# Kernel optimization log

Hardware: AMD Instinct MI355X
Metric: run time of the kernel (lower is better)

The kernel has to match this reference:

```python
import jax, jax.numpy as jnp
import numpy as np

N_NODES = 100000
N_EDGES = 1280000
N_REL = 8
DIM = 64
N_LAYERS = 2
N_TGT = 50000


def setup_inputs() -> dict:
    key = jax.random.key(0)
    ks = jax.random.split(key, 8)
    x_idx = jnp.arange(N_NODES, dtype=jnp.int64) if jax.config.jax_enable_x64 else jnp.arange(N_NODES, dtype=jnp.int32)
    edge_index = jax.random.randint(ks[0], (2, N_EDGES), 0, N_NODES)
    edge_type = jax.random.randint(ks[1], (N_EDGES,), 0, N_REL)
    target_edge_index = jax.random.randint(ks[2], (2, N_TGT), 0, N_NODES)
    # xavier-ish scales to keep activations stable through relu stack
    node_emb = jax.random.normal(ks[3], (N_NODES, DIM), dtype=jnp.float32) * 0.1
    weight = jax.random.normal(ks[4], (N_LAYERS, N_REL, DIM, DIM), dtype=jnp.float32) * (1.0 / np.sqrt(DIM))
    root = jax.random.normal(ks[5], (N_LAYERS, DIM, DIM), dtype=jnp.float32) * (1.0 / np.sqrt(DIM))
    bias = jax.random.normal(ks[6], (N_LAYERS, DIM), dtype=jnp.float32) * 0.01
    return {"x_idx": x_idx, "edge_index": edge_index, "edge_type": edge_type,
            "target_edge_index": target_edge_index, "node_emb": node_emb,
            "weight": weight, "root": root, "bias": bias}


def reference(x_idx, edge_index, edge_type, target_edge_index, node_emb, weight, root, bias):
    # RGCN forward: x = node_emb[x_idx]; L x (FastRGCNConv + relu); edge dot-product score.
    x = node_emb[x_idx]                       # [N, D]
    src, dst = edge_index[0], edge_index[1]   # messages flow src -> dst (PyG source_to_target)
    n = x.shape[0]
    # in-degree for 'mean' aggregation (zero-degree nodes get 0, guard div)
    deg = jax.ops.segment_sum(jnp.ones((src.shape[0],), dtype=x.dtype), dst, num_segments=n)
    inv_deg = (1.0 / jnp.maximum(deg, 1.0))[:, None]  # [N, 1]
    n_layers = weight.shape[0]
    for l in range(n_layers):
        # transform every node by every relation, then gather per edge (FastRGCNConv math)
        h = jnp.einsum('ni,rio->rno', x, weight[l])   # [R, N, D]
        msg = h[edge_type, src]                       # [E, D]
        agg = jax.ops.segment_sum(msg, dst, num_segments=n) * inv_deg  # mean aggr [N, D]
        x = jax.nn.relu(agg + x @ root[l] + bias[l])
    s, t = target_edge_index[0], target_edge_index[1]
    return jnp.sum(x[s] * x[t], axis=-1)              # [T]
```

## Files before the change

### kernel.cpp

```cpp
#include <hip/hip_runtime.h>
#include <hip/hip_bf16.h>

#define DIM 64
#define NREL 8
#define KTOT 576

typedef __bf16 bf16x8 __attribute__((ext_vector_type(8)));
typedef __bf16 bf16x4 __attribute__((ext_vector_type(4)));
typedef float  f32x4  __attribute__((ext_vector_type(4)));

__global__ __launch_bounds__(256) void histgather_kernel(const int* __restrict__ dst,
                                                         const int* __restrict__ et,
                                                         int* __restrict__ deg8,
                                                         int* __restrict__ eoff,
                                                         const int* __restrict__ x_idx,
                                                         const float* __restrict__ emb,
                                                         __bf16* __restrict__ xb0,
                                                         __bf16* __restrict__ hbuf,
                                                         int* __restrict__ srcs,
                                                         int N, int E, int epad_cap) {
    int i = blockIdx.x * 256 + threadIdx.x;
    if (i < N * DIM) {
        int n = i >> 6;
        int c = i & 63;
        xb0[i] = (__bf16)emb[(size_t)x_idx[n] * DIM + c];
    }
    if (i < DIM) {
        hbuf[(size_t)N * NREL * DIM + i] = (__bf16)0.f;
    }
    if (i < epad_cap) srcs[i] = N * NREL;
    if (i < E) eoff[i] = atomicAdd(&deg8[dst[i] * 8 + et[i]], 1);
}

__global__ __launch_bounds__(256) void scan1_kernel(const int* __restrict__ deg8,
                                                    int* __restrict__ offs,
                                                    int* __restrict__ bsum,
                                                    float* __restrict__ invdeg, int N) {
    __shared__ int sd[256];
    int tid = threadIdx.x;
    int d = blockIdx.x * 256 + tid;
    int vpad = 0;
    if (d < N) {
        int vtrue = 0;
#pragma unroll
        for (int r = 0; r < NREL; ++r) vtrue += deg8[d * 8 + r];
        vpad = (vtrue + 3) & ~3;
        invdeg[d] = 1.0f / fmaxf((float)vtrue, 1.0f);
    }
    sd[tid] = vpad;
    __syncthreads();
#pragma unroll
    for (int off = 1; off < 256; off <<= 1) {
        int t = (tid >= off) ? sd[tid - off] : 0;
        __syncthreads();
        sd[tid] += t;
        __syncthreads();
    }
    if (d < N) offs[d] = sd[tid] - vpad;
    if (tid == 255) bsum[blockIdx.x] = sd[255];
}

__global__ __launch_bounds__(512) void scan2wcat_kernel(int* __restrict__ bsum, int nb,
                                                        const float* __restrict__ weight,
                                                        const float* __restrict__ root,
                                                        __bf16* __restrict__ Wt2, int L) {
    if (blockIdx.x == 0) {
        __shared__ int sd[512];
        int tid = threadIdx.x;
        int v = (tid < nb) ? bsum[tid] : 0;
        sd[tid] = v;
        __syncthreads();
#pragma unroll
        for (int off = 1; off < 512; off <<= 1) {
            int t = (tid >= off) ? sd[tid - off] : 0;
            __syncthreads();
            sd[tid] += t;
            __syncthreads();
        }
        if (tid < nb) bsum[tid] = sd[tid] - v;
    } else {
        int idx = (blockIdx.x - 1) * 512 + threadIdx.x;
        int total = L * KTOT * DIM;
        if (idx >= total) return;
        int l = idx / (KTOT * DIM);
        int rem = idx - l * (KTOT * DIM);
        int row = rem / DIM;
        int ch = rem - row * DIM;
        float w;
        if (row < 512) {
            int r = row >> 6, c = row & 63;
            w = weight[(((l * 8 + r) * 64) + ch) * 64 + c];
        } else {
            w = root[(l * 64 + ch) * 64 + (row - 512)];
        }
        Wt2[idx] = (__bf16)w;
    }
}

__global__ __launch_bounds__(256) void rpbuild_kernel(const int* __restrict__ deg8,
                                                      const int* __restrict__ offs,
                                                      const int* __restrict__ bsum,
                                                      int* __restrict__ rp,
                                                      int N) {
    int d = blockIdx.x * 256 + threadIdx.x;
    if (d >= N) return;
    int base = offs[d] + bsum[blockIdx.x];
    int run = 0;
#pragma unroll
    for (int r = 0; r < NREL; ++r) {
        rp[d * 8 + r] = base + run;
        run += deg8[d * 8 + r];
    }
    if (d == N - 1) rp[(size_t)N * 8] = base + ((run + 3) & ~3);
}

__global__ __launch_bounds__(256) void bucket_kernel(const int* __restrict__ src,
                                                     const int* __restrict__ dst,
                                                     const int* __restrict__ et,
                                                     const int* __restrict__ rp,
                                                     const int* __restrict__ eoff,
                                                     int* __restrict__ srcs, int E) {
    int i = blockIdx.x * 256 + threadIdx.x;
    int half = (E + 1) >> 1;
    if (i >= half) return;
    int iB = i + half;
    bool hasB = iB < E;
    int etA = et[i];
    int etB = hasB ? et[iB] : 0;
    int cellA = dst[i] * 8 + etA;
    int cellB = hasB ? dst[iB] * 8 + etB : 0;
    int rA = rp[cellA];
    int rB = hasB ? rp[cellB] : 0;
    int oA = eoff[i];
    int oB = hasB ? eoff[iB] : 0;
    int sA = src[i];
    int sB = hasB ? src[iB] : 0;
    srcs[rA + oA] = sA * NREL + etA;
    if (hasB) srcs[rB + oB] = sB * NREL + etB;
}

__global__ __launch_bounds__(256) void transform_kernel(const __bf16* __restrict__ xin,
                                                        const __bf16* __restrict__ Wt2,
                                                        __bf16* __restrict__ h, int N) {
    int wave = threadIdx.x >> 6;
    int lane = threadIdx.x & 63;
    int l15 = lane & 15;
    int lg  = lane >> 4;

    bf16x8 afrag[8][2];
#pragma unroll
    for (int p = 0; p < 8; ++p) {
        const __bf16* wrow = Wt2 + (size_t)(p * 64 + 16 * wave + l15) * DIM + lg * 8;
        afrag[p][0] = *reinterpret_cast<const bf16x8*>(wrow);
        afrag[p][1] = *reinterpret_cast<const bf16x8*>(wrow + 32);
    }
    int cb = 16 * wave + 4 * lg;

    int ntiles = (N + 15) >> 4;
    for (int tile = blockIdx.x; tile < ntiles; tile += gridDim.x) {
        int n = tile * 16 + l15;
        int nc = (n < N) ? n : (N - 1);
        const __bf16* xrow = xin + (size_t)nc * DIM + lg * 8;
        bf16x8 bv0 = *reinterpret_cast<const bf16x8*>(xrow);
        bf16x8 bv1 = *reinterpret_cast<const bf16x8*>(xrow + 32);

#pragma unroll
        for (int p = 0; p < 8; ++p) {
            f32x4 acc = (f32x4){0.f, 0.f, 0.f, 0.f};
            acc = __builtin_amdgcn_mfma_f32_16x16x32_bf16(afrag[p][0], bv0, acc, 0, 0, 0);
            acc = __builtin_amdgcn_mfma_f32_16x16x32_bf16(afrag[p][1], bv1, acc, 0, 0, 0);
            if (n < N) {
                bf16x4 hv;
#pragma unroll
                for (int i = 0; i < 4; ++i) hv[i] = (__bf16)acc[i];
                *reinterpret_cast<bf16x4*>(h + (size_t)n * (NREL * DIM) + p * 64 + cb) = hv;
            }
        }
    }
}

__global__ __launch_bounds__(256) void aggroot_kernel(const __bf16* __restrict__ h,
                                                      const __bf16* __restrict__ xin,
                                                      const int* __restrict__ srcs,
                                                      const int* __restrict__ rp,
                                                      const float* __restrict__ invdeg,
                                                      const __bf16* __restrict__ Wt2,
                                                      const float* __restrict__ bias_l,
                                                      __bf16* __restrict__ xout, int N) {
    __shared__ __align__(16) float S16[16][68];
    int wave = threadIdx.x >> 6;
    int lane = threadIdx.x & 63;
    int l15 = lane & 15;
    int lg  = lane >> 4;
    const int SENT = N * NREL;

    bf16x8 ar0, ar1;
    {
        const __bf16* wrow = Wt2 + (size_t)(512 + 16 * wave + l15) * DIM + lg * 8;
        ar0 = *reinterpret_cast<const bf16x8*>(wrow);
        ar1 = *reinterpret_cast<const bf16x8*>(wrow + 32);
    }
    int cbase = 16 * wave + 4 * lg;
    f32x4 bias4 = *reinterpret_cast<const f32x4*>(bias_l + cbase);

    int tile = blockIdx.x;

#pragma unroll
    for (int rr = 0; rr < 4; ++rr) {
        int d0 = tile * 16 + wave * 4 + rr;
        if (d0 >= N) d0 = N - 1;
        int d = __builtin_amdgcn_readfirstlane(d0);
        int qb = rp[d * 8];
        int qe = rp[d * 8 + 8];
        float acc = 0.f;
        for (int q = qb; q < qe; q += 16) {
            int rem = qe - q;
            int4 sa = *reinterpret_cast<const int4*>(srcs + q);
            int4 sb = *reinterpret_cast<const int4*>(srcs + q + 4);
            int4 sc = *reinterpret_cast<const int4*>(srcs + q + 8);
            int4 sd = *reinterpret_cast<const int4*>(srcs + q + 12);
            bool vb = rem >= 8, vc = rem >= 12, vd = rem >= 16;
            int i0 = sa.x,              i1 = sa.y,              i2 = sa.z,              i3 = sa.w;
            int i4 = vb ? sb.x : SENT,  i5 = vb ? sb.y : SENT,  i6 = vb ? sb.z : SENT,  i7 = vb ? sb.w : SENT;
            int i8 = vc ? sc.x : SENT,  i9 = vc ? sc.y : SENT,  iA = vc ? sc.z : SENT,  iB = vc ? sc.w : SENT;
            int iC = vd ? sd.x : SENT,  iD = vd ? sd.y : SENT,  iE = vd ? sd.z : SENT,  iF = vd ? sd.w : SENT;
            float v0 = (float)h[(size_t)i0 * DIM + lane];
            float v1 = (float)h[(size_t)i1 * DIM + lane];
            float v2 = (float)h[(size_t)i2 * DIM + lane];
            float v3 = (float)h[(size_t)i3 * DIM + lane];
            float v4 = (float)h[(size_t)i4 * DIM + lane];
            float v5 = (float)h[(size_t)i5 * DIM + lane];
            float v6 = (float)h[(size_t)i6 * DIM + lane];
            float v7 = (float)h[(size_t)i7 * DIM + lane];
            float v8 = (float)h[(size_t)i8 * DIM + lane];
            float v9 = (float)h[(size_t)i9 * DIM + lane];
            float vA = (float)h[(size_t)iA * DIM + lane];
            float vB = (float)h[(size_t)iB * DIM + lane];
            float vC = (float)h[(size_t)iC * DIM + lane];
            float vD = (float)h[(size_t)iD * DIM + lane];
            float vE = (float)h[(size_t)iE * DIM + lane];
            float vF = (float)h[(size_t)iF * DIM + lane];
            acc += (((v0 + v1) + (v2 + v3)) + ((v4 + v5) + (v6 + v7)))
                 + (((v8 + v9) + (vA + vB)) + ((vC + vD) + (vE + vF)));
        }
        S16[wave * 4 + rr][lane] = acc * invdeg[d];
    }
    __syncthreads();

    int n = tile * 16 + l15;
    int nc = (n < N) ? n : (N - 1);
    const __bf16* xrow = xin + (size_t)nc * DIM + lg * 8;
    bf16x8 bv0 = *reinterpret_cast<const bf16x8*>(xrow);
    bf16x8 bv1 = *reinterpret_cast<const bf16x8*>(xrow + 32);
    f32x4 acc = (f32x4){0.f, 0.f, 0.f, 0.f};
    acc = __builtin_amdgcn_mfma_f32_16x16x32_bf16(ar0, bv0, acc, 0, 0, 0);
    acc = __builtin_amdgcn_mfma_f32_16x16x32_bf16(ar1, bv1, acc, 0, 0, 0);

    if (n < N) {
        f32x4 ag = *reinterpret_cast<const f32x4*>(&S16[l15][cbase]);
        bf16x4 hv;
#pragma unroll
        for (int i = 0; i < 4; ++i)
            hv[i] = (__bf16)fmaxf(acc[i] + ag[i] + bias4[i], 0.f);
        *reinterpret_cast<bf16x4*>(xout + (size_t)n * DIM + cbase) = hv;
    }
}

__global__ __launch_bounds__(256) void score_kernel(const __bf16* __restrict__ xb,
                                                    const int* __restrict__ s,
                                                    const int* __restrict__ t,
                                                    float* __restrict__ out, int T) {
    int i = blockIdx.x * 4 + (threadIdx.x >> 6);
    if (i >= T) return;
    int lane = threadIdx.x & 63;
    float p = (float)xb[(size_t)s[i] * DIM + lane] * (float)xb[(size_t)t[i] * DIM + lane];
#pragma unroll
    for (int off = 32; off > 0; off >>= 1) p += __shfl_down(p, off, 64);
    if (lane == 0) out[i] = p;
}

extern "C" void kernel_launch(void* const* d_in, const int* in_sizes, int n_in,
                              void* d_out, int out_size, void* d_ws, size_t ws_size,
                              hipStream_t stream) {
    const int*   x_idx  = (const int*)d_in[0];
    const int*   eidx   = (const int*)d_in[1];
    const int*   etyp   = (const int*)d_in[2];
    const int*   tidx   = (const int*)d_in[3];
    const float* emb    = (const float*)d_in[4];
    const float* weight = (const float*)d_in[5];
    const float* root   = (const float*)d_in[6];
    const float* bias   = (const float*)d_in[7];

    int N = in_sizes[0];
    int E = in_sizes[2];
    int T = in_sizes[3] / 2;
    int L = in_sizes[5] / (NREL * DIM * DIM);

    const int* src = eidx;
    const int* dst = eidx + E;
    const int* ts  = tidx;
    const int* tt  = tidx + T;
    float* out = (float*)d_out;

    int epad_cap = E + 3 * N + 64;

    char* p = (char*)d_ws;
    auto alloc = [&](size_t bytes) -> void* {
        void* r = (void*)p;
        p += (bytes + 255) & ~(size_t)255;
        return r;
    };
    __bf16* hbuf    = (__bf16*)alloc(((size_t)N * NREL + 1) * DIM * sizeof(__bf16));
    __bf16* xb0     = (__bf16*)alloc((size_t)N * DIM * sizeof(__bf16));
    __bf16* xb1     = (__bf16*)alloc((size_t)N * DIM * sizeof(__bf16));
    __bf16* Wt2     = (__bf16*)alloc((size_t)L * KTOT * DIM * sizeof(__bf16));
    int*    srcs    = (int*)   alloc((size_t)epad_cap * sizeof(int));
    int*    eoff    = (int*)   alloc((size_t)E * sizeof(int));
    int*    deg8    = (int*)   alloc((size_t)N * 8 * sizeof(int));
    int*    rp      = (int*)   alloc(((size_t)N * 8 + 1) * sizeof(int));
    int*    offs    = (int*)   alloc((size_t)N * sizeof(int));
    float*  invdeg  = (float*) alloc((size_t)N * sizeof(float));
    int*    bsum    = (int*)   alloc(1024 * sizeof(int));

    int nb = (N + 255) / 256;
    int ntiles = (N + 15) / 16;

    hipMemsetAsync(deg8, 0, (size_t)N * 8 * sizeof(int), stream);
    histgather_kernel<<<((size_t)N * DIM + 255) / 256, 256, 0, stream>>>(
        dst, etyp, deg8, eoff, x_idx, emb, xb0, hbuf, srcs, N, E, epad_cap);
    scan1_kernel<<<nb, 256, 0, stream>>>(deg8, offs, bsum, invdeg, N);
    {
        int wtotal = L * KTOT * DIM;
        int wblocks = 1 + (wtotal + 511) / 512;
        scan2wcat_kernel<<<wblocks, 512, 0, stream>>>(bsum, nb, weight, root, Wt2, L);
    }
    rpbuild_kernel<<<nb, 256, 0, stream>>>(deg8, offs, bsum, rp, N);
    {
        int half = (E + 1) / 2;
        bucket_kernel<<<(half + 255) / 256, 256, 0, stream>>>(src, dst, etyp, rp, eoff, srcs, E);
    }

    __bf16* xcur = xb0;
    __bf16* xnxt = xb1;
    for (int l = 0; l < L; ++l) {
        transform_kernel<<<2048, 256, 0, stream>>>(xcur, Wt2 + (size_t)l * KTOT * DIM, hbuf, N);
        aggroot_kernel<<<ntiles, 256, 0, stream>>>(hbuf, xcur, srcs, rp, invdeg,
                                                   Wt2 + (size_t)l * KTOT * DIM,
                                                   bias + (size_t)l * DIM,
                                                   xnxt, N);
        __bf16* tmp = xcur; xcur = xnxt; xnxt = tmp;
    }

    score_kernel<<<(T + 3) / 4, 256, 0, stream>>>(xcur, ts, tt, out, T);
}
```

Baseline: 361.3 us.

## Merge scan, weight concat, row-pointer build and bucketing into one cooperative kernel

Replaces four preprocessing launches (block scan, top-level scan plus weight conversion, row-pointer build, edge bucketing) with a single cooperative kernel that uses grid-wide syncs between phases. Scan blocks grow to 512 threads so the 196 block sums fit one block scan. The aim is to cut kernel launch gaps and tail idle time. The cost is that bucketing now runs on only about 196 blocks with grid-stride loops, which may lower memory parallelism for 1.28M scattered writes, and grid.sync itself has overhead.

```diff
diff --git a/kernel.cpp b/kernel.cpp
--- a/kernel.cpp
+++ b/kernel.cpp
@@ -1,5 +1,8 @@
 #include <hip/hip_runtime.h>
 #include <hip/hip_bf16.h>
+#include <hip/hip_cooperative_groups.h>
+
+namespace cg = cooperative_groups;
 
 #define DIM 64
 #define NREL 8
@@ -32,13 +35,25 @@
     if (i < E) eoff[i] = atomicAdd(&deg8[dst[i] * 8 + et[i]], 1);
 }
 
-__global__ __launch_bounds__(256) void scan1_kernel(const int* __restrict__ deg8,
-                                                    int* __restrict__ offs,
-                                                    int* __restrict__ bsum,
-                                                    float* __restrict__ invdeg, int N) {
-    __shared__ int sd[256];
+__global__ __launch_bounds__(512) void prep_kernel(const int* __restrict__ deg8,
+                                                   int* __restrict__ offs,
+                                                   int* __restrict__ bsum,
+                                                   float* __restrict__ invdeg,
+                                                   const float* __restrict__ weight,
+                                                   const float* __restrict__ root,
+                                                   __bf16* __restrict__ Wt2,
+                                                   int* __restrict__ rp,
+                                                   const int* __restrict__ esrc,
+                                                   const int* __restrict__ edst,
+                                                   const int* __restrict__ eet,
+                                                   const int* __restrict__ eoff,
+                                                   int* __restrict__ srcs,
+                                                   int N, int E, int L, int nb2) {
+    cg::grid_group grid = cg::this_grid();
+    __shared__ int sd[512];
     int tid = threadIdx.x;
-    int d = blockIdx.x * 256 + tid;
+    int d = blockIdx.x * 512 + tid;
+
     int vpad = 0;
     if (d < N) {
         int vtrue = 0;
@@ -50,24 +65,36 @@
     sd[tid] = vpad;
     __syncthreads();
 #pragma unroll
-    for (int off = 1; off < 256; off <<= 1) {
+    for (int off = 1; off < 512; off <<= 1) {
         int t = (tid >= off) ? sd[tid - off] : 0;
         __syncthreads();
         sd[tid] += t;
         __syncthreads();
     }
     if (d < N) offs[d] = sd[tid] - vpad;
-    if (tid == 255) bsum[blockIdx.x] = sd[255];
-}
-
-__global__ __launch_bounds__(512) void scan2wcat_kernel(int* __restrict__ bsum, int nb,
-                                                        const float* __restrict__ weight,
-                                                        const float* __restrict__ root,
-                                                        __bf16* __restrict__ Wt2, int L) {
+    if (tid == 511) bsum[blockIdx.x] = sd[511];
+
+    {
+        int total = L * KTOT * DIM;
+        for (int idx = blockIdx.x * 512 + tid; idx < total; idx += gridDim.x * 512) {
+            int l = idx / (KTOT * DIM);
+            int rem = idx - l * (KTOT * DIM);
+            int row = rem / DIM;
+            int ch = rem - row * DIM;
+            float w;
+            if (row < 512) {
+                int r = row >> 6, c = row & 63;
+                w = weight[(((l * 8 + r) * 64) + ch) * 64 + c];
+            } else {
+                w = root[(l * 64 + ch) * 64 + (row - 512)];
+            }
+            Wt2[idx] = (__bf16)w;
+        }
+    }
+    grid.sync();
+
     if (blockIdx.x == 0) {
-        __shared__ int sd[512];
-        int tid = threadIdx.x;
-        int v = (tid < nb) ? bsum[tid] : 0;
+        int v = (tid < nb2) ? bsum[tid] : 0;
         sd[tid] = v;
         __syncthreads();
 #pragma unroll
@@ -77,66 +104,42 @@
             sd[tid] += t;
             __syncthreads();
         }
-        if (tid < nb) bsum[tid] = sd[tid] - v;
-    } else {
-        int idx = (blockIdx.x - 1) * 512 + threadIdx.x;
-        int total = L * KTOT * DIM;
-        if (idx >= total) return;
-        int l = idx / (KTOT * DIM);
-        int rem = idx - l * (KTOT * DIM);
-        int row = rem / DIM;
-        int ch = rem - row * DIM;
-        float w;
-        if (row < 512) {
-            int r = row >> 6, c = row & 63;
-            w = weight[(((l * 8 + r) * 64) + ch) * 64 + c];
-        } else {
-            w = root[(l * 64 + ch) * 64 + (row - 512)];
-        }
-        Wt2[idx] = (__bf16)w;
-    }
-}
-
-__global__ __launch_bounds__(256) void rpbuild_kernel(const int* __restrict__ deg8,
-                                                      const int* __restrict__ offs,
-                                                      const int* __restrict__ bsum,
-                                                      int* __restrict__ rp,
-                                                      int N) {
-    int d = blockIdx.x * 256 + threadIdx.x;
-    if (d >= N) return;
-    int base = offs[d] + bsum[blockIdx.x];
-    int run = 0;
-#pragma unroll
-    for (int r = 0; r < NREL; ++r) {
-        rp[d * 8 + r] = base + run;
-        run += deg8[d * 8 + r];
-    }
-    if (d == N - 1) rp[(size_t)N * 8] = base + ((run + 3) & ~3);
-}
-
-__global__ __launch_bounds__(256) void bucket_kernel(const int* __restrict__ src,
-                                                     const int* __restrict__ dst,
-                                                     const int* __restrict__ et,
-                                                     const int* __restrict__ rp,
-                                                     const int* __restrict__ eoff,
-                                                     int* __restrict__ srcs, int E) {
-    int i = blockIdx.x * 256 + threadIdx.x;
-    int half = (E + 1) >> 1;
-    if (i >= half) return;
-    int iB = i + half;
-    bool hasB = iB < E;
-    int etA = et[i];
-    int etB = hasB ? et[iB] : 0;
-    int cellA = dst[i] * 8 + etA;
-    int cellB = hasB ? dst[iB] * 8 + etB : 0;
-    int rA = rp[cellA];
-    int rB = hasB ? rp[cellB] : 0;
-    int oA = eoff[i];
-    int oB = hasB ? eoff[iB] : 0;
-    int sA = src[i];
-    int sB = hasB ? src[iB] : 0;
-    srcs[rA + oA] = sA * NREL + etA;
-    if (hasB) srcs[rB + oB] = sB * NREL + etB;
+        if (tid < nb2) bsum[tid] = sd[tid] - v;
+    }
+    grid.sync();
+
+    if (d < N) {
+        int base = offs[d] + bsum[blockIdx.x];
+        int run = 0;
+#pragma unroll
+        for (int r = 0; r < NREL; ++r) {
+            rp[d * 8 + r] = base + run;
+            run += deg8[d * 8 + r];
+        }
+        if (d == N - 1) rp[(size_t)N * 8] = base + ((run + 3) & ~3);
+    }
+    grid.sync();
+
+    {
+        int half = (E + 1) >> 1;
+        int stride = gridDim.x * 512;
+        for (int i = blockIdx.x * 512 + tid; i < half; i += stride) {
+            int iB = i + half;
+            bool hasB = iB < E;
+            int etA = eet[i];
+            int etB = hasB ? eet[iB] : 0;
+            int cellA = edst[i] * 8 + etA;
+            int cellB = hasB ? edst[iB] * 8 + etB : 0;
+            int rA = rp[cellA];
+            int rB = hasB ? rp[cellB] : 0;
+            int oA = eoff[i];
+            int oB = hasB ? eoff[iB] : 0;
+            int sA = esrc[i];
+            int sB = hasB ? esrc[iB] : 0;
+            srcs[rA + oA] = sA * NREL + etA;
+            if (hasB) srcs[rB + oB] = sB * NREL + etB;
+        }
+    }
 }
 
 __global__ __launch_bounds__(256) void transform_kernel(const __bf16* __restrict__ xin,
@@ -322,22 +325,20 @@
     float*  invdeg  = (float*) alloc((size_t)N * sizeof(float));
     int*    bsum    = (int*)   alloc(1024 * sizeof(int));
 
-    int nb = (N + 255) / 256;
+    int nb2 = (N + 511) / 512;
     int ntiles = (N + 15) / 16;
 
     hipMemsetAsync(deg8, 0, (size_t)N * 8 * sizeof(int), stream);
     histgather_kernel<<<((size_t)N * DIM + 255) / 256, 256, 0, stream>>>(
         dst, etyp, deg8, eoff, x_idx, emb, xb0, hbuf, srcs, N, E, epad_cap);
-    scan1_kernel<<<nb, 256, 0, stream>>>(deg8, offs, bsum, invdeg, N);
+
     {
-        int wtotal = L * KTOT * DIM;
-        int wblocks = 1 + (wtotal + 511) / 512;
-        scan2wcat_kernel<<<wblocks, 512, 0, stream>>>(bsum, nb, weight, root, Wt2, L);
-    }
-    rpbuild_kernel<<<nb, 256, 0, stream>>>(deg8, offs, bsum, rp, N);
-    {
-        int half = (E + 1) / 2;
-        bucket_kernel<<<(half + 255) / 256, 256, 0, stream>>>(src, dst, etyp, rp, eoff, srcs, E);
+        void* args[] = { (void*)&deg8, (void*)&offs, (void*)&bsum, (void*)&invdeg,
+                         (void*)&weight, (void*)&root, (void*)&Wt2, (void*)&rp,
+                         (void*)&src, (void*)&dst, (void*)&etyp, (void*)&eoff,
+                         (void*)&srcs, (void*)&N, (void*)&E, (void*)&L, (void*)&nb2 };
+        hipLaunchCooperativeKernel((const void*)prep_kernel, dim3(nb2), dim3(512),
+                                   args, 0, stream);
     }
 
     __bf16* xcur = xb0;
```

After: 450.2 us. +24.6%, slower.

## Fuse layer transform, aggregation and scoring into one persistent cooperative kernel

Applied to the files above, without the earlier changes.

Replaces the per-layer transform and aggregate kernels and the score kernel with a single cooperative persistent kernel. Grid-wide syncs separate the phases, and blocks loop over tiles with a grid-stride. The aim is to remove several launch gaps and tail effects. In exchange, the grid is capped at 1024 blocks, each grid.sync costs something, and the aggregation phase now grid-strides with fewer blocks, which may reduce latency hiding for the irregular gathers.

```diff
diff --git a/kernel.cpp b/kernel.cpp
--- a/kernel.cpp
+++ b/kernel.cpp
@@ -1,5 +1,8 @@
 #include <hip/hip_runtime.h>
 #include <hip/hip_bf16.h>
+#include <hip/hip_cooperative_groups.h>
+
+namespace cg = cooperative_groups;
 
 #define DIM 64
 #define NREL 8
@@ -139,144 +142,147 @@
     if (hasB) srcs[rB + oB] = sB * NREL + etB;
 }
 
-__global__ __launch_bounds__(256) void transform_kernel(const __bf16* __restrict__ xin,
-                                                        const __bf16* __restrict__ Wt2,
-                                                        __bf16* __restrict__ h, int N) {
-    int wave = threadIdx.x >> 6;
-    int lane = threadIdx.x & 63;
-    int l15 = lane & 15;
-    int lg  = lane >> 4;
-
-    bf16x8 afrag[8][2];
-#pragma unroll
-    for (int p = 0; p < 8; ++p) {
-        const __bf16* wrow = Wt2 + (size_t)(p * 64 + 16 * wave + l15) * DIM + lg * 8;
-        afrag[p][0] = *reinterpret_cast<const bf16x8*>(wrow);
-        afrag[p][1] = *reinterpret_cast<const bf16x8*>(wrow + 32);
-    }
-    int cb = 16 * wave + 4 * lg;
-
-    int ntiles = (N + 15) >> 4;
-    for (int tile = blockIdx.x; tile < ntiles; tile += gridDim.x) {
-        int n = tile * 16 + l15;
-        int nc = (n < N) ? n : (N - 1);
-        const __bf16* xrow = xin + (size_t)nc * DIM + lg * 8;
-        bf16x8 bv0 = *reinterpret_cast<const bf16x8*>(xrow);
-        bf16x8 bv1 = *reinterpret_cast<const bf16x8*>(xrow + 32);
-
-#pragma unroll
-        for (int p = 0; p < 8; ++p) {
-            f32x4 acc = (f32x4){0.f, 0.f, 0.f, 0.f};
-            acc = __builtin_amdgcn_mfma_f32_16x16x32_bf16(afrag[p][0], bv0, acc, 0, 0, 0);
-            acc = __builtin_amdgcn_mfma_f32_16x16x32_bf16(afrag[p][1], bv1, acc, 0, 0, 0);
-            if (n < N) {
-                bf16x4 hv;
-#pragma unroll
-                for (int i = 0; i < 4; ++i) hv[i] = (__bf16)acc[i];
-                *reinterpret_cast<bf16x4*>(h + (size_t)n * (NREL * DIM) + p * 64 + cb) = hv;
-            }
-        }
-    }
-}
-
-__global__ __launch_bounds__(256) void aggroot_kernel(const __bf16* __restrict__ h,
-                                                      const __bf16* __restrict__ xin,
-                                                      const int* __restrict__ srcs,
-                                                      const int* __restrict__ rp,
-                                                      const float* __restrict__ invdeg,
-                                                      const __bf16* __restrict__ Wt2,
-                                                      const float* __restrict__ bias_l,
-                                                      __bf16* __restrict__ xout, int N) {
+__global__ __launch_bounds__(256) void layers_kernel(__bf16* __restrict__ xb0,
+                                                     __bf16* __restrict__ xb1,
+                                                     __bf16* __restrict__ hbuf,
+                                                     const int* __restrict__ srcs,
+                                                     const int* __restrict__ rp,
+                                                     const float* __restrict__ invdeg,
+                                                     const __bf16* __restrict__ Wt2,
+                                                     const float* __restrict__ bias,
+                                                     const int* __restrict__ ts,
+                                                     const int* __restrict__ tt,
+                                                     float* __restrict__ out,
+                                                     int N, int T, int L) {
+    cg::grid_group grid = cg::this_grid();
     __shared__ __align__(16) float S16[16][68];
     int wave = threadIdx.x >> 6;
     int lane = threadIdx.x & 63;
     int l15 = lane & 15;
     int lg  = lane >> 4;
     const int SENT = N * NREL;
-
-    bf16x8 ar0, ar1;
-    {
-        const __bf16* wrow = Wt2 + (size_t)(512 + 16 * wave + l15) * DIM + lg * 8;
-        ar0 = *reinterpret_cast<const bf16x8*>(wrow);
-        ar1 = *reinterpret_cast<const bf16x8*>(wrow + 32);
-    }
-    int cbase = 16 * wave + 4 * lg;
-    f32x4 bias4 = *reinterpret_cast<const f32x4*>(bias_l + cbase);
-
-    int tile = blockIdx.x;
-
-#pragma unroll
-    for (int rr = 0; rr < 4; ++rr) {
-        int d0 = tile * 16 + wave * 4 + rr;
-        if (d0 >= N) d0 = N - 1;
-        int d = __builtin_amdgcn_readfirstlane(d0);
-        int qb = rp[d * 8];
-        int qe = rp[d * 8 + 8];
-        float acc = 0.f;
-        for (int q = qb; q < qe; q += 16) {
-            int rem = qe - q;
-            int4 sa = *reinterpret_cast<const int4*>(srcs + q);
-            int4 sb = *reinterpret_cast<const int4*>(srcs + q + 4);
-            int4 sc = *reinterpret_cast<const int4*>(srcs + q + 8);
-            int4 sd = *reinterpret_cast<const int4*>(srcs + q + 12);
-            bool vb = rem >= 8, vc = rem >= 12, vd = rem >= 16;
-            int i0 = sa.x,              i1 = sa.y,              i2 = sa.z,              i3 = sa.w;
-            int i4 = vb ? sb.x : SENT,  i5 = vb ? sb.y : SENT,  i6 = vb ? sb.z : SENT,  i7 = vb ? sb.w : SENT;
-            int i8 = vc ? sc.x : SENT,  i9 = vc ? sc.y : SENT,  iA = vc ? sc.z : SENT,  iB = vc ? sc.w : SENT;
-            int iC = vd ? sd.x : SENT,  iD = vd ? sd.y : SENT,  iE = vd ? sd.z : SENT,  iF = vd ? sd.w : SENT;
-            float v0 = (float)h[(size_t)i0 * DIM + lane];
-            float v1 = (float)h[(size_t)i1 * DIM + lane];
-            float v2 = (float)h[(size_t)i2 * DIM + lane];
-            float v3 = (float)h[(size_t)i3 * DIM + lane];
-            float v4 = (float)h[(size_t)i4 * DIM + lane];
-            float v5 = (float)h[(size_t)i5 * DIM + lane];
-            float v6 = (float)h[(size_t)i6 * DIM + lane];
-            float v7 = (float)h[(size_t)i7 * DIM + lane];
-            float v8 = (float)h[(size_t)i8 * DIM + lane];
-            float v9 = (float)h[(size_t)i9 * DIM + lane];
-            float vA = (float)h[(size_t)iA * DIM + lane];
-            float vB = (float)h[(size_t)iB * DIM + lane];
-            float vC = (float)h[(size_t)iC * DIM + lane];
-            float vD = (float)h[(size_t)iD * DIM + lane];
-            float vE = (float)h[(size_t)iE * DIM + lane];
-            float vF = (float)h[(size_t)iF * DIM + lane];
-            acc += (((v0 + v1) + (v2 + v3)) + ((v4 + v5) + (v6 + v7)))
-                 + (((v8 + v9) + (vA + vB)) + ((vC + vD) + (vE + vF)));
+    int ntiles = (N + 15) >> 4;
+
+    __bf16* xcur = xb0;
+    __bf16* xnxt = xb1;
+    for (int l = 0; l < L; ++l) {
+        const __bf16* Wl = Wt2 + (size_t)l * KTOT * DIM;
+
+        {
+            bf16x8 afrag[8][2];
+#pragma unroll
+            for (int p = 0; p < 8; ++p) {
+                const __bf16* wrow = Wl + (size_t)(p * 64 + 16 * wave + l15) * DIM + lg * 8;
+                afrag[p][0] = *reinterpret_cast<const bf16x8*>(wrow);
+                afrag[p][1] = *reinterpret_cast<const bf16x8*>(wrow + 32);
+            }
+            int cb = 16 * wave + 4 * lg;
+            for (int tile = blockIdx.x; tile < ntiles; tile += gridDim.x) {
+                int n = tile * 16 + l15;
+                int nc = (n < N) ? n : (N - 1);
+                const __bf16* xrow = xcur + (size_t)nc * DIM + lg * 8;
+                bf16x8 bv0 = *reinterpret_cast<const bf16x8*>(xrow);
+                bf16x8 bv1 = *reinterpret_cast<const bf16x8*>(xrow + 32);
+#pragma unroll
+                for (int p = 0; p < 8; ++p) {
+                    f32x4 acc = (f32x4){0.f, 0.f, 0.f, 0.f};
+                    acc = __builtin_amdgcn_mfma_f32_16x16x32_bf16(afrag[p][0], bv0, acc, 0, 0, 0);
+                    acc = __builtin_amdgcn_mfma_f32_16x16x32_bf16(afrag[p][1], bv1, acc, 0, 0, 0);
+                    if (n < N) {
+                        bf16x4 hv;
+#pragma unroll
+                        for (int i = 0; i < 4; ++i) hv[i] = (__bf16)acc[i];
+                        *reinterpret_cast<bf16x4*>(hbuf + (size_t)n * (NREL * DIM) + p * 64 + cb) = hv;
+                    }
+                }
+            }
         }
-        S16[wave * 4 + rr][lane] = acc * invdeg[d];
-    }
-    __syncthreads();
-
-    int n = tile * 16 + l15;
-    int nc = (n < N) ? n : (N - 1);
-    const __bf16* xrow = xin + (size_t)nc * DIM + lg * 8;
-    bf16x8 bv0 = *reinterpret_cast<const bf16x8*>(xrow);
-    bf16x8 bv1 = *reinterpret_cast<const bf16x8*>(xrow + 32);
-    f32x4 acc = (f32x4){0.f, 0.f, 0.f, 0.f};
-    acc = __builtin_amdgcn_mfma_f32_16x16x32_bf16(ar0, bv0, acc, 0, 0, 0);
-    acc = __builtin_amdgcn_mfma_f32_16x16x32_bf16(ar1, bv1, acc, 0, 0, 0);
-
-    if (n < N) {
-        f32x4 ag = *reinterpret_cast<const f32x4*>(&S16[l15][cbase]);
-        bf16x4 hv;
-#pragma unroll
-        for (int i = 0; i < 4; ++i)
-            hv[i] = (__bf16)fmaxf(acc[i] + ag[i] + bias4[i], 0.f);
-        *reinterpret_cast<bf16x4*>(xout + (size_t)n * DIM + cbase) = hv;
-    }
-}
-
-__global__ __launch_bounds__(256) void score_kernel(const __bf16* __restrict__ xb,
-                                                    const int* __restrict__ s,
-                                                    const int* __restrict__ t,
-                                                    float* __restrict__ out, int T) {
-    int i = blockIdx.x * 4 + (threadIdx.x >> 6);
-    if (i >= T) return;
-    int lane = threadIdx.x & 63;
-    float p = (float)xb[(size_t)s[i] * DIM + lane] * (float)xb[(size_t)t[i] * DIM + lane];
-#pragma unroll
-    for (int off = 32; off > 0; off >>= 1) p += __shfl_down(p, off, 64);
-    if (lane == 0) out[i] = p;
+        grid.sync();
+
+        {
+            bf16x8 ar0, ar1;
+            {
+                const __bf16* wrow = Wl + (size_t)(512 + 16 * wave + l15) * DIM + lg * 8;
+                ar0 = *reinterpret_cast<const bf16x8*>(wrow);
+                ar1 = *reinterpret_cast<const bf16x8*>(wrow + 32);
+            }
+            int cbase = 16 * wave + 4 * lg;
+            f32x4 bias4 = *reinterpret_cast<const f32x4*>(bias + (size_t)l * DIM + cbase);
+
+            for (int tile = blockIdx.x; tile < ntiles; tile += gridDim.x) {
+#pragma unroll
+                for (int rr = 0; rr < 4; ++rr) {
+                    int d0 = tile * 16 + wave * 4 + rr;
+                    if (d0 >= N) d0 = N - 1;
+                    int d = __builtin_amdgcn_readfirstlane(d0);
+                    int qb = rp[d * 8];
+                    int qe = rp[d * 8 + 8];
+                    float acc = 0.f;
+                    for (int q = qb; q < qe; q += 16) {
+                        int rem = qe - q;
+                        int4 sa = *reinterpret_cast<const int4*>(srcs + q);
+                        int4 sb = *reinterpret_cast<const int4*>(srcs + q + 4);
+                        int4 sc = *reinterpret_cast<const int4*>(srcs + q + 8);
+                        int4 sd = *reinterpret_cast<const int4*>(srcs + q + 12);
+                        bool vb = rem >= 8, vc = rem >= 12, vd = rem >= 16;
+                        int i0 = sa.x,             i1 = sa.y,             i2 = sa.z,             i3 = sa.w;
+                        int i4 = vb ? sb.x : SENT, i5 = vb ? sb.y : SENT, i6 = vb ? sb.z : SENT, i7 = vb ? sb.w : SENT;
+                        int i8 = vc ? sc.x : SENT, i9 = vc ? sc.y : SENT, iA = vc ? sc.z : SENT, iB = vc ? sc.w : SENT;
+                        int iC = vd ? sd.x : SENT, iD = vd ? sd.y : SENT, iE = vd ? sd.z : SENT, iF = vd ? sd.w : SENT;
+                        float v0 = (float)hbuf[(size_t)i0 * DIM + lane];
+                        float v1 = (float)hbuf[(size_t)i1 * DIM + lane];
+                        float v2 = (float)hbuf[(size_t)i2 * DIM + lane];
+                        float v3 = (float)hbuf[(size_t)i3 * DIM + lane];
+                        float v4 = (float)hbuf[(size_t)i4 * DIM + lane];
+                        float v5 = (float)hbuf[(size_t)i5 * DIM + lane];
+                        float v6 = (float)hbuf[(size_t)i6 * DIM + lane];
+                        float v7 = (float)hbuf[(size_t)i7 * DIM + lane];
+                        float v8 = (float)hbuf[(size_t)i8 * DIM + lane];
+                        float v9 = (float)hbuf[(size_t)i9 * DIM + lane];
+                        float vA = (float)hbuf[(size_t)iA * DIM + lane];
+                        float vB = (float)hbuf[(size_t)iB * DIM + lane];
+                        float vC = (float)hbuf[(size_t)iC * DIM + lane];
+                        float vD = (float)hbuf[(size_t)iD * DIM + lane];
+                        float vE = (float)hbuf[(size_t)iE * DIM + lane];
+                        float vF = (float)hbuf[(size_t)iF * DIM + lane];
+                        acc += (((v0 + v1) + (v2 + v3)) + ((v4 + v5) + (v6 + v7)))
+                             + (((v8 + v9) + (vA + vB)) + ((vC + vD) + (vE + vF)));
+                    }
+                    S16[wave * 4 + rr][lane] = acc * invdeg[d];
+                }
+                __syncthreads();
+
+                int n = tile * 16 + l15;
+                int nc = (n < N) ? n : (N - 1);
+                const __bf16* xrow = xcur + (size_t)nc * DIM + lg * 8;
+                bf16x8 bv0 = *reinterpret_cast<const bf16x8*>(xrow);
+                bf16x8 bv1 = *reinterpret_cast<const bf16x8*>(xrow + 32);
+                f32x4 acc = (f32x4){0.f, 0.f, 0.f, 0.f};
+                acc = __builtin_amdgcn_mfma_f32_16x16x32_bf16(ar0, bv0, acc, 0, 0, 0);
+                acc = __builtin_amdgcn_mfma_f32_16x16x32_bf16(ar1, bv1, acc, 0, 0, 0);
+
+                if (n < N) {
+                    f32x4 ag = *reinterpret_cast<const f32x4*>(&S16[l15][cbase]);
+                    bf16x4 hv;
+#pragma unroll
+                    for (int i = 0; i < 4; ++i)
+                        hv[i] = (__bf16)fmaxf(acc[i] + ag[i] + bias4[i], 0.f);
+                    *reinterpret_cast<bf16x4*>(xnxt + (size_t)n * DIM + cbase) = hv;
+                }
+                __syncthreads();
+            }
+        }
+        grid.sync();
+
+        __bf16* tmp = xcur; xcur = xnxt; xnxt = tmp;
+    }
+
+    for (int i = blockIdx.x * 4 + wave; i < T; i += gridDim.x * 4) {
+        float p = (float)xcur[(size_t)ts[i] * DIM + lane] * (float)xcur[(size_t)tt[i] * DIM + lane];
+#pragma unroll
+        for (int off = 32; off > 0; off >>= 1) p += __shfl_down(p, off, 64);
+        if (lane == 0) out[i] = p;
+    }
 }
 
 extern "C" void kernel_launch(void* const* d_in, const int* in_sizes, int n_in,
@@ -323,7 +329,6 @@
     int*    bsum    = (int*)   alloc(1024 * sizeof(int));
 
     int nb = (N + 255) / 256;
-    int ntiles = (N + 15) / 16;
 
     hipMemsetAsync(deg8, 0, (size_t)N * 8 * sizeof(int), stream);
     histgather_kernel<<<((size_t)N * DIM + 255) / 256, 256, 0, stream>>>(
@@ -340,16 +345,17 @@
         bucket_kernel<<<(half + 255) / 256, 256, 0, stream>>>(src, dst, etyp, rp, eoff, srcs, E);
     }
 
-    __bf16* xcur = xb0;
-    __bf16* xnxt = xb1;
-    for (int l = 0; l < L; ++l) {
-        transform_kernel<<<2048, 256, 0, stream>>>(xcur, Wt2 + (size_t)l * KTOT * DIM, hbuf, N);
-        aggroot_kernel<<<ntiles, 256, 0, stream>>>(hbuf, xcur, srcs, rp, invdeg,
-                                                   Wt2 + (size_t)l * KTOT * DIM,
-                                                   bias + (size_t)l * DIM,
-                                                   xnxt, N);
-        __bf16* tmp = xcur; xcur = xnxt; xnxt = tmp;
-    }
-
-    score_kernel<<<(T + 3) / 4, 256, 0, stream>>>(xcur, ts, tt, out, T);
-}
+    {
+        int bpc = 0;
+        hipOccupancyMaxActiveBlocksPerMultiprocessor(&bpc, (const void*)layers_kernel, 256, 0);
+        if (bpc < 1) bpc = 1;
+        int grid = bpc * 256;
+        if (grid > 1024) grid = 1024;
+        void* args[] = { (void*)&xb0, (void*)&xb1, (void*)&hbuf, (void*)&srcs,
+                         (void*)&rp, (void*)&invdeg, (void*)&Wt2, (void*)&bias,
+                         (void*)&ts, (void*)&tt, (void*)&out,
+                         (void*)&N, (void*)&T, (void*)&L };
+        hipLaunchCooperativeKernel((const void*)layers_kernel, dim3(grid), dim3(256),
+                                   args, 0, stream);
+    }
+}
```

New measurement: 708.9 us. 96.2% more time.

## Fuse block scan, block-sum scan, row-pointer build and weight cast into one kernel

Applied to the files above, without the earlier changes.

Replaces the three-kernel scan (per-block scan, block-sum scan with weight conversion, row-pointer build) with one kernel. Each block takes its base offset from a global atomic counter instead of an ordered prefix over block sums, and writes per-node end offsets in a new array so consumers no longer rely on contiguous rp ordering. This drops two launches and the offs/bsum round trips. In exchange, node segment order in the srcs array becomes nondeterministic across blocks, and the weight cast is done with a grid-stride loop.

```diff
diff --git a/kernel.cpp b/kernel.cpp
--- a/kernel.cpp
+++ b/kernel.cpp
@@ -32,18 +32,25 @@
     if (i < E) eoff[i] = atomicAdd(&deg8[dst[i] * 8 + et[i]], 1);
 }
 
-__global__ __launch_bounds__(256) void scan1_kernel(const int* __restrict__ deg8,
-                                                    int* __restrict__ offs,
-                                                    int* __restrict__ bsum,
-                                                    float* __restrict__ invdeg, int N) {
+__global__ __launch_bounds__(256) void scan1rp_kernel(const int* __restrict__ deg8,
+                                                      int* __restrict__ gtotal,
+                                                      float* __restrict__ invdeg,
+                                                      int* __restrict__ rp,
+                                                      int* __restrict__ rend,
+                                                      const float* __restrict__ weight,
+                                                      const float* __restrict__ root,
+                                                      __bf16* __restrict__ Wt2,
+                                                      int N, int L) {
     __shared__ int sd[256];
+    __shared__ int sbase;
     int tid = threadIdx.x;
     int d = blockIdx.x * 256 + tid;
+    int dv[NREL];
     int vpad = 0;
     if (d < N) {
         int vtrue = 0;
 #pragma unroll
-        for (int r = 0; r < NREL; ++r) vtrue += deg8[d * 8 + r];
+        for (int r = 0; r < NREL; ++r) { dv[r] = deg8[d * 8 + r]; vtrue += dv[r]; }
         vpad = (vtrue + 3) & ~3;
         invdeg[d] = 1.0f / fmaxf((float)vtrue, 1.0f);
     }
@@ -56,32 +63,20 @@
         sd[tid] += t;
         __syncthreads();
     }
-    if (d < N) offs[d] = sd[tid] - vpad;
-    if (tid == 255) bsum[blockIdx.x] = sd[255];
-}
-
-__global__ __launch_bounds__(512) void scan2wcat_kernel(int* __restrict__ bsum, int nb,
-                                                        const float* __restrict__ weight,
-                                                        const float* __restrict__ root,
-                                                        __bf16* __restrict__ Wt2, int L) {
-    if (blockIdx.x == 0) {
-        __shared__ int sd[512];
-        int tid = threadIdx.x;
-        int v = (tid < nb) ? bsum[tid] : 0;
-        sd[tid] = v;
-        __syncthreads();
-#pragma unroll
-        for (int off = 1; off < 512; off <<= 1) {
-            int t = (tid >= off) ? sd[tid - off] : 0;
-            __syncthreads();
-            sd[tid] += t;
-            __syncthreads();
+    if (tid == 255) sbase = atomicAdd(gtotal, sd[255]);
+    __syncthreads();
+    if (d < N) {
+        int base = sbase + sd[tid] - vpad;
+        int run = 0;
+#pragma unroll
+        for (int r = 0; r < NREL; ++r) {
+            rp[d * 8 + r] = base + run;
+            run += dv[r];
         }
-        if (tid < nb) bsum[tid] = sd[tid] - v;
-    } else {
-        int idx = (blockIdx.x - 1) * 512 + threadIdx.x;
-        int total = L * KTOT * DIM;
-        if (idx >= total) return;
+        rend[d] = base + vpad;
+    }
+    int total = L * KTOT * DIM;
+    for (int idx = blockIdx.x * 256 + tid; idx < total; idx += gridDim.x * 256) {
         int l = idx / (KTOT * DIM);
         int rem = idx - l * (KTOT * DIM);
         int row = rem / DIM;
@@ -95,23 +90,6 @@
         }
         Wt2[idx] = (__bf16)w;
     }
-}
-
-__global__ __launch_bounds__(256) void rpbuild_kernel(const int* __restrict__ deg8,
-                                                      const int* __restrict__ offs,
-                                                      const int* __restrict__ bsum,
-                                                      int* __restrict__ rp,
-                                                      int N) {
-    int d = blockIdx.x * 256 + threadIdx.x;
-    if (d >= N) return;
-    int base = offs[d] + bsum[blockIdx.x];
-    int run = 0;
-#pragma unroll
-    for (int r = 0; r < NREL; ++r) {
-        rp[d * 8 + r] = base + run;
-        run += deg8[d * 8 + r];
-    }
-    if (d == N - 1) rp[(size_t)N * 8] = base + ((run + 3) & ~3);
 }
 
 __global__ __launch_bounds__(256) void bucket_kernel(const int* __restrict__ src,
@@ -183,6 +161,7 @@
                                                       const __bf16* __restrict__ xin,
                                                       const int* __restrict__ srcs,
                                                       const int* __restrict__ rp,
+                                                      const int* __restrict__ rend,
                                                       const float* __restrict__ invdeg,
                                                       const __bf16* __restrict__ Wt2,
                                                       const float* __restrict__ bias_l,
@@ -211,7 +190,7 @@
         if (d0 >= N) d0 = N - 1;
         int d = __builtin_amdgcn_readfirstlane(d0);
         int qb = rp[d * 8];
-        int qe = rp[d * 8 + 8];
+        int qe = rend[d];
         float acc = 0.f;
         for (int q = qb; q < qe; q += 16) {
             int rem = qe - q;
@@ -316,25 +295,21 @@
     __bf16* Wt2     = (__bf16*)alloc((size_t)L * KTOT * DIM * sizeof(__bf16));
     int*    srcs    = (int*)   alloc((size_t)epad_cap * sizeof(int));
     int*    eoff    = (int*)   alloc((size_t)E * sizeof(int));
-    int*    deg8    = (int*)   alloc((size_t)N * 8 * sizeof(int));
-    int*    rp      = (int*)   alloc(((size_t)N * 8 + 1) * sizeof(int));
-    int*    offs    = (int*)   alloc((size_t)N * sizeof(int));
+    int*    deg8    = (int*)   alloc(((size_t)N * 8 + 8) * sizeof(int));
+    int*    rp      = (int*)   alloc((size_t)N * 8 * sizeof(int));
+    int*    rend    = (int*)   alloc((size_t)N * sizeof(int));
     float*  invdeg  = (float*) alloc((size_t)N * sizeof(float));
-    int*    bsum    = (int*)   alloc(1024 * sizeof(int));
+
+    int* gtotal = deg8 + (size_t)N * 8;
 
     int nb = (N + 255) / 256;
     int ntiles = (N + 15) / 16;
 
-    hipMemsetAsync(deg8, 0, (size_t)N * 8 * sizeof(int), stream);
+    hipMemsetAsync(deg8, 0, ((size_t)N * 8 + 8) * sizeof(int), stream);
     histgather_kernel<<<((size_t)N * DIM + 255) / 256, 256, 0, stream>>>(
         dst, etyp, deg8, eoff, x_idx, emb, xb0, hbuf, srcs, N, E, epad_cap);
-    scan1_kernel<<<nb, 256, 0, stream>>>(deg8, offs, bsum, invdeg, N);
-    {
-        int wtotal = L * KTOT * DIM;
-        int wblocks = 1 + (wtotal + 511) / 512;
-        scan2wcat_kernel<<<wblocks, 512, 0, stream>>>(bsum, nb, weight, root, Wt2, L);
-    }
-    rpbuild_kernel<<<nb, 256, 0, stream>>>(deg8, offs, bsum, rp, N);
+    scan1rp_kernel<<<nb, 256, 0, stream>>>(deg8, gtotal, invdeg, rp, rend,
+                                           weight, root, Wt2, N, L);
     {
         int half = (E + 1) / 2;
         bucket_kernel<<<(half + 255) / 256, 256, 0, stream>>>(src, dst, etyp, rp, eoff, srcs, E);
@@ -344,7 +319,7 @@
     __bf16* xnxt = xb1;
     for (int l = 0; l < L; ++l) {
         transform_kernel<<<2048, 256, 0, stream>>>(xcur, Wt2 + (size_t)l * KTOT * DIM, hbuf, N);
-        aggroot_kernel<<<ntiles, 256, 0, stream>>>(hbuf, xcur, srcs, rp, invdeg,
+        aggroot_kernel<<<ntiles, 256, 0, stream>>>(hbuf, xcur, srcs, rp, rend, invdeg,
                                                    Wt2 + (size_t)l * KTOT * DIM,
                                                    bias + (size_t)l * DIM,
                                                    xnxt, N);
```

After: 355.1 us. No clear change (-1.7%).
